# Kernel optimization log

Hardware: AMD Instinct MI355X
Metric: run time of the kernel (lower is better)

Reference implementation:

```python
import jax, jax.numpy as jnp
import numpy as np

# ---- static configuration (from init_kwargs) ----
L = 36.0            # cubic cell edge (bohr)
G = 180             # grid points per axis
NA = 64             # number of atoms
NRAD = 8            # basis['n']
NL = 4              # basis['l']
RO = 2.5            # basis['r_o'] (bohr)
A = L / G           # grid spacing (orthorhombic -> U = diag(A))
RMAX = int(np.ceil(RO / A))          # half-width of periodic box (13)
B = 2 * RMAX + 1                     # box edge (27)
VCELL = A ** 3                       # |det U|
# static coefficient mask: keep (n,l,m) with |m - NL| <= l  (same as tril*flip(tril))
_MASK = np.abs(np.arange(2 * NL + 1)[None, :] - NL) <= np.arange(NL)[:, None]


def _make_W():
    # orthonormalization matrix W = S^{-1/2} for radials phi_n(r) = r^2 (r_o - r)^{n+2}
    r = np.linspace(0.0, RO, 4000)
    phi = np.stack([r ** 2 * (RO - r) ** (n + 2) for n in range(NRAD)])
    S = np.trapz(phi[:, None] * phi[None, :], r, axis=-1)
    w, v = np.linalg.eigh(S)
    return (v @ np.diag(w ** -0.5) @ v.T).astype(np.float32)


def setup_inputs() -> dict:
    key = jax.random.key(0)
    k1, k2 = jax.random.split(key)
    rho = jax.random.uniform(k1, (G, G, G), dtype=jnp.float32)       # electron density >= 0
    positions = jax.random.uniform(k2, (NA, 3), dtype=jnp.float32) * L
    return {"rho": rho, "positions": positions, "W": jnp.asarray(_make_W())}


def _sph_padded(theta, phi):
    # real spherical harmonics, zero-padded to [NL, 2*NL+1, ...] with m at index NL+m
    ct = jnp.cos(theta); st = jnp.sin(theta)
    cp = jnp.cos(phi); sp = jnp.sin(phi)
    c2p = jnp.cos(2 * phi); s2p = jnp.sin(2 * phi)
    c3p = jnp.cos(3 * phi); s3p = jnp.sin(3 * phi)
    z = jnp.zeros_like(theta)
    one = jnp.ones_like(theta)
    Y = {
        (0, 0): 0.28209479177387814 * one,
        (1, -1): 0.4886025119029199 * st * sp,
        (1, 0): 0.4886025119029199 * ct,
        (1, 1): 0.4886025119029199 * st * cp,
        (2, -2): 0.5462742152960396 * st ** 2 * s2p,
        (2, -1): 1.0925484305920792 * st * ct * sp,
        (2, 0): 0.31539156525252005 * (3 * ct ** 2 - 1),
        (2, 1): 1.0925484305920792 * st * ct * cp,
        (2, 2): 0.5462742152960396 * st ** 2 * c2p,
        (3, -3): 0.5900435899266435 * st ** 3 * s3p,
        (3, -2): 1.445305721320277 * st ** 2 * ct * s2p,
        (3, -1): 0.4570457994644658 * st * (5 * ct ** 2 - 1) * sp,
        (3, 0): 0.3731763325901154 * (5 * ct ** 3 - 3 * ct),
        (3, 1): 0.4570457994644658 * st * (5 * ct ** 2 - 1) * cp,
        (3, 2): 1.445305721320277 * st ** 2 * ct * c2p,
        (3, 3): 0.5900435899266435 * st ** 3 * c3p,
    }
    rows = []
    for l in range(NL):
        pad = [z] * (NL - l)
        rows.append(jnp.stack(pad + [Y[(l, m)] for m in range(-l, l + 1)] + pad))
    return jnp.stack(rows)  # [NL, 2NL+1, B, B, B]


def _project_atom(rho, pos, W):
    a = jnp.float32(A)
    cm = jnp.round(pos / a)            # nearest grid index of atom (U_inv @ pos)
    dr = pos - a * cm                  # sub-grid displacement
    offs = jnp.arange(-RMAX, RMAX + 1, dtype=jnp.float32)
    # periodic mesh indices (box_around / fmod wrap)
    Xm = jnp.mod(offs + cm[0], G).astype(jnp.int32)
    Ym = jnp.mod(offs + cm[1], G).astype(jnp.int32)
    Zm = jnp.mod(offs + cm[2], G).astype(jnp.int32)
    srho = rho[Xm[:, None, None], Ym[None, :, None], Zm[None, None, :]]  # [B,B,B] gather
    # euclidean coords relative to the atom
    Xs = (offs * a - dr[0])[:, None, None]
    Ys = (offs * a - dr[1])[None, :, None]
    Zs = (offs * a - dr[2])[None, None, :]
    Xs, Ys, Zs = jnp.broadcast_arrays(Xs, Ys, Zs)
    R = jnp.sqrt(Xs ** 2 + Ys ** 2 + Zs ** 2)
    Rsafe = jnp.where(R < 1e-12, 1.0, R)
    Theta = jnp.where(R < 1e-12, 0.0, jnp.arccos(jnp.clip(Zs / Rsafe, -1.0, 1.0)))
    Phi = jnp.arctan2(Ys, Xs)
    angs = _sph_padded(Theta, Phi)                       # [NL, 2NL+1, B,B,B]
    ns = jnp.arange(NRAD, dtype=jnp.float32)[:, None, None, None]
    phi_n = jnp.where(R < RO, R ** 2 * jnp.maximum(RO - R, 0.0) ** (ns + 2.0), 0.0)
    rads = jnp.einsum('nm,mijk->nijk', W, phi_n) * jnp.float32(VCELL)  # [NRAD, B,B,B]
    coeff = jnp.einsum('lmijk,nijk,ijk->nlm', angs, rads, srho)        # [NRAD, NL, 2NL+1]
    return coeff[:, _MASK].reshape(-1)                    # [NRAD * NL^2] = 128


def reference(rho, positions, W):
    # vmap over atoms (single species -> identical box shape per atom)
    return jax.vmap(lambda p: _project_atom(rho, p, W))(positions)  # [NA, 128]
```

## Files before the change

### kernel.cpp

```cpp
#include <hip/hip_runtime.h>

#define G 180
#define NRAD 8
#define RO_F 2.5f
#define A_F 0.2f
#define VCELL_F 0.008f
#define CELLS 19683
#define SLABS 8
#define NATOMS 64



__global__ __launch_bounds__(256, 4) void proj_kernel(
    const float* __restrict__ rho, const float* __restrict__ pos,
    float* __restrict__ ws)
{
    const int atom = blockIdx.y;
    const int slab = blockIdx.x;
    const int tid  = threadIdx.x;
    const int lane = tid & 63;
    const int w    = tid >> 6;

    const float px = pos[atom*3+0], py = pos[atom*3+1], pz = pos[atom*3+2];
    const float cmx = rintf(px * 5.0f), cmy = rintf(py * 5.0f), cmz = rintf(pz * 5.0f);
    const float drx = px - A_F*cmx, dry = py - A_F*cmy, drz = pz - A_F*cmz;
    const int icx = (int)cmx - 13, icy = (int)cmy - 13, icz = (int)cmz - 13;

    float acc[32];
    #pragma unroll
    for (int j = 0; j < 32; ++j) acc[j] = 0.0f;

    for (int c = slab*64 + lane; c < CELLS; c += SLABS*64) {
        int i = c / 729;
        int rem = c - i*729;
        int j = rem / 27;
        int k = rem - j*27;
        int gx = i + icx; gx += (gx < 0) ? G : 0; gx -= (gx >= G) ? G : 0;
        int gy = j + icy; gy += (gy < 0) ? G : 0; gy -= (gy >= G) ? G : 0;
        int gz = k + icz; gz += (gz < 0) ? G : 0; gz -= (gz >= G) ? G : 0;
        float s = rho[(gx*G + gy)*G + gz];

        float x = (float)(i-13)*A_F - drx;
        float y = (float)(j-13)*A_F - dry;
        float z = (float)(k-13)*A_F - drz;
        float r2 = x*x + y*y + z*z;
        float inv = rsqrtf(fmaxf(r2, 1e-24f));
        float R = r2 * inv;
        if (R < RO_F) {
            float t = RO_F - R;
            float ux = x*inv, uy = y*inv, uz = z*inv;
            float uz2 = uz*uz;
            float ux2 = ux*ux, uy2 = uy*uy;
            float ys[16];
            ys[0]  = 0.28209479177f;
            ys[1]  = 0.48860251190f * uy;
            ys[2]  = 0.48860251190f * uz;
            ys[3]  = 0.48860251190f * ux;
            ys[4]  = 1.09254843059f * ux*uy;
            ys[5]  = 1.09254843059f * uy*uz;
            ys[6]  = 0.31539156525f * (3.0f*uz2 - 1.0f);
            ys[7]  = 1.09254843059f * ux*uz;
            ys[8]  = 0.54627421530f * (ux2 - uy2);
            ys[9]  = 0.59004358993f * uy*(3.0f*ux2 - uy2);
            ys[10] = 2.89061144264f * ux*uy*uz;
            ys[11] = 0.45704579946f * uy*(5.0f*uz2 - 1.0f);
            ys[12] = 0.37317633259f * uz*(5.0f*uz2 - 3.0f);
            ys[13] = 0.45704579946f * ux*(5.0f*uz2 - 1.0f);
            ys[14] = 1.44530572132f * (ux2 - uy2)*uz;
            ys[15] = 0.59004358993f * ux*(ux2 - 3.0f*uy2);

            float t2 = t*t;
            float p = s * r2 * t2;
            if (w >= 1) p *= t2;
            if (w >= 2) p *= t2;
            if (w >= 3) p *= t2;
            float pt = p * t;
            #pragma unroll
            for (int q = 0; q < 16; ++q) {
                acc[q]    = fmaf(p,  ys[q], acc[q]);
                acc[16+q] = fmaf(pt, ys[q], acc[16+q]);
            }
        }
    }

    __shared__ float red[4][64][33];
    __shared__ float stage[4][2][32];
    #pragma unroll
    for (int q = 0; q < 32; ++q)
        red[w][lane][q] = acc[q];
    __syncthreads();
    const int col  = lane & 31;
    const int half = lane >> 5;
    float csum = 0.0f;
    #pragma unroll
    for (int r = 0; r < 32; ++r)
        csum += red[w][half*32 + r][col];
    stage[w][half][col] = csum;
    __syncthreads();
    if (lane < 32) {
        float v = stage[w][0][lane] + stage[w][1][lane];
        ws[((atom*SLABS + slab)*4 + w)*32 + lane] = v;
    }
}

__global__ void finalize_kernel(const float* __restrict__ ws,
                                const float* __restrict__ W,
                                float* __restrict__ out)
{
    const int atom = blockIdx.x;
    const int t = threadIdx.x;
    const int n = t >> 4, q = t & 15;
    const float* base = ws + atom*SLABS*4*32;
    float M[8];
    #pragma unroll
    for (int k = 0; k < 8; ++k) {
        const int g = k >> 1, row = k & 1;
        float sk = 0.0f;
        #pragma unroll
        for (int s = 0; s < 8; ++s)
            sk += base[(s*4 + g)*32 + row*16 + q];
        M[k] = sk;
    }
    float sum = 0.0f;
    #pragma unroll
    for (int k = 0; k < 8; ++k)
        sum = fmaf(W[n*8+k], M[k], sum);
    out[atom*128 + t] = sum * VCELL_F;
}

extern "C" void kernel_launch(void* const* d_in, const int* in_sizes, int n_in,
                              void* d_out, int out_size, void* d_ws, size_t ws_size,
                              hipStream_t stream) {
    const float* rho = (const float*)d_in[0];
    const float* pos = (const float*)d_in[1];
    const float* W   = (const float*)d_in[2];
    float* out = (float*)d_out;
    float* ws  = (float*)d_ws;

    dim3 grid(SLABS, NATOMS);
    proj_kernel<<<grid, 256, 0, stream>>>(rho, pos, ws);
    finalize_kernel<<<NATOMS, 128, 0, stream>>>(ws, W, out);
}
```

Before: 88.85 us.

## Give each wave four radial powers, double slabs, and prefetch rho in a fixed loop

Each wave now accumulates four consecutive radial powers (64 accumulators) instead of two, so the cell spans are split across two waves per power group. This halves the redundant spherical-harmonic and distance work per cell. The slab count doubles and the loop becomes a fixed 10-iteration loop that software-prefetches the next rho value. Cells past the box end are left to the R < RO test to zero out. The LDS reduction drops its block barriers and relies on per-wave lockstep, and the finalize kernel is reworked for the new workspace layout. The cost is higher register pressure, with the occupancy hint lowered from 4 to 3.

```diff
diff --git a/kernel.cpp b/kernel.cpp
--- a/kernel.cpp
+++ b/kernel.cpp
@@ -6,12 +6,12 @@
 #define A_F 0.2f
 #define VCELL_F 0.008f
 #define CELLS 19683
-#define SLABS 8
+#define SLABS 16
 #define NATOMS 64
+#define ITERS 10
 
 
-
-__global__ __launch_bounds__(256, 4) void proj_kernel(
+__global__ __launch_bounds__(256, 3) void proj_kernel(
     const float* __restrict__ rho, const float* __restrict__ pos,
     float* __restrict__ ws)
 {
@@ -20,25 +20,42 @@
     const int tid  = threadIdx.x;
     const int lane = tid & 63;
     const int w    = tid >> 6;
+    const int g    = w >> 1;
+    const int cw   = w & 1;
 
     const float px = pos[atom*3+0], py = pos[atom*3+1], pz = pos[atom*3+2];
     const float cmx = rintf(px * 5.0f), cmy = rintf(py * 5.0f), cmz = rintf(pz * 5.0f);
     const float drx = px - A_F*cmx, dry = py - A_F*cmy, drz = pz - A_F*cmz;
     const int icx = (int)cmx - 13, icy = (int)cmy - 13, icz = (int)cmz - 13;
 
-    float acc[32];
+    float acc[64];
     #pragma unroll
-    for (int j = 0; j < 32; ++j) acc[j] = 0.0f;
+    for (int j = 0; j < 64; ++j) acc[j] = 0.0f;
 
-    for (int c = slab*64 + lane; c < CELLS; c += SLABS*64) {
-        int i = c / 729;
-        int rem = c - i*729;
-        int j = rem / 27;
-        int k = rem - j*27;
+    int c = slab*128 + cw*64 + lane;
+
+    int i_n, j_n, k_n; float s_n;
+    {
+        int i = c / 729; int rem = c - i*729; int j = rem / 27; int k = rem - j*27;
         int gx = i + icx; gx += (gx < 0) ? G : 0; gx -= (gx >= G) ? G : 0;
         int gy = j + icy; gy += (gy < 0) ? G : 0; gy -= (gy >= G) ? G : 0;
         int gz = k + icz; gz += (gz < 0) ? G : 0; gz -= (gz >= G) ? G : 0;
-        float s = rho[(gx*G + gy)*G + gz];
+        i_n = i; j_n = j; k_n = k;
+        s_n = rho[(gx*G + gy)*G + gz];
+    }
+
+    for (int it = 0; it < ITERS; ++it) {
+        const int i = i_n, j = j_n, k = k_n;
+        const float s = s_n;
+        c += SLABS*128;
+        if (it != ITERS-1) {
+            int i2 = c / 729; int rem = c - i2*729; int j2 = rem / 27; int k2 = rem - j2*27;
+            int gx = i2 + icx; gx += (gx < 0) ? G : 0; gx -= (gx >= G) ? G : 0;
+            int gy = j2 + icy; gy += (gy < 0) ? G : 0; gy -= (gy >= G) ? G : 0;
+            int gz = k2 + icz; gz += (gz < 0) ? G : 0; gz -= (gz >= G) ? G : 0;
+            i_n = i2; j_n = j2; k_n = k2;
+            s_n = rho[(gx*G + gy)*G + gz];
+        }
 
         float x = (float)(i-13)*A_F - drx;
         float y = (float)(j-13)*A_F - dry;
@@ -70,36 +87,37 @@
             ys[15] = 0.59004358993f * ux*(ux2 - 3.0f*uy2);
 
             float t2 = t*t;
-            float p = s * r2 * t2;
-            if (w >= 1) p *= t2;
-            if (w >= 2) p *= t2;
-            if (w >= 3) p *= t2;
-            float pt = p * t;
+            float p0 = s * r2 * t2;
+            if (g) { float t4 = t2*t2; p0 *= t4; }
+            float p1 = p0*t, p2 = p1*t, p3 = p2*t;
             #pragma unroll
             for (int q = 0; q < 16; ++q) {
-                acc[q]    = fmaf(p,  ys[q], acc[q]);
-                acc[16+q] = fmaf(pt, ys[q], acc[16+q]);
+                acc[q]    = fmaf(p0, ys[q], acc[q]);
+                acc[16+q] = fmaf(p1, ys[q], acc[16+q]);
+                acc[32+q] = fmaf(p2, ys[q], acc[32+q]);
+                acc[48+q] = fmaf(p3, ys[q], acc[48+q]);
             }
         }
     }
 
     __shared__ float red[4][64][33];
     __shared__ float stage[4][2][32];
-    #pragma unroll
-    for (int q = 0; q < 32; ++q)
-        red[w][lane][q] = acc[q];
-    __syncthreads();
     const int col  = lane & 31;
     const int half = lane >> 5;
-    float csum = 0.0f;
     #pragma unroll
-    for (int r = 0; r < 32; ++r)
-        csum += red[w][half*32 + r][col];
-    stage[w][half][col] = csum;
-    __syncthreads();
-    if (lane < 32) {
-        float v = stage[w][0][lane] + stage[w][1][lane];
-        ws[((atom*SLABS + slab)*4 + w)*32 + lane] = v;
+    for (int ch = 0; ch < 2; ++ch) {
+        #pragma unroll
+        for (int q = 0; q < 32; ++q)
+            red[w][lane][q] = acc[ch*32 + q];
+        float csum = 0.0f;
+        #pragma unroll
+        for (int r = 0; r < 32; ++r)
+            csum += red[w][half*32 + r][col];
+        stage[w][half][col] = csum;
+        if (lane < 32) {
+            float v = stage[w][0][lane] + stage[w][1][lane];
+            ws[((atom*SLABS + slab)*4 + w)*64 + ch*32 + lane] = v;
+        }
     }
 }
 
@@ -110,21 +128,21 @@
     const int atom = blockIdx.x;
     const int t = threadIdx.x;
     const int n = t >> 4, q = t & 15;
-    const float* base = ws + atom*SLABS*4*32;
-    float M[8];
+    const int g = n >> 2, r = n & 3;
+    const float* base = ws + atom*SLABS*4*64;
+    float m = 0.0f;
     #pragma unroll
-    for (int k = 0; k < 8; ++k) {
-        const int g = k >> 1, row = k & 1;
-        float sk = 0.0f;
-        #pragma unroll
-        for (int s = 0; s < 8; ++s)
-            sk += base[(s*4 + g)*32 + row*16 + q];
-        M[k] = sk;
+    for (int s = 0; s < SLABS; ++s) {
+        m += base[(s*4 + g*2 + 0)*64 + r*16 + q];
+        m += base[(s*4 + g*2 + 1)*64 + r*16 + q];
     }
+    __shared__ float M[8][16];
+    M[n][q] = m;
+    __syncthreads();
     float sum = 0.0f;
     #pragma unroll
     for (int k = 0; k < 8; ++k)
-        sum = fmaf(W[n*8+k], M[k], sum);
+        sum = fmaf(W[n*8+k], M[k][q], sum);
     out[atom*128 + t] = sum * VCELL_F;
 }
 
```

After: 80.23 us. 1.11x faster.
